# Performance work log

Hardware: AMD Instinct MI355X
Metric: run time of the kernel (lower is better)

## Reference

```python
import jax, jax.numpy as jnp
import numpy as np

B, L, D, H, DH, DI, NL, V = 1, 2048, 1024, 16, 64, 4096, 12, 32000
EPS = 1e-5  # torch LayerNorm default eps
SCALE = 1.0 / DH ** 0.5


def _ln(x):
    # LayerNorm with elementwise_affine=False
    m = jnp.mean(x, axis=-1, keepdims=True)
    va = jnp.var(x, axis=-1, keepdims=True)
    return (x - m) / jnp.sqrt(va + EPS)


def setup_inputs() -> dict:
    key = jax.random.key(0)
    ks = jax.random.split(key, 12)
    s = 0.02
    return {
        "X": jax.random.randint(ks[0], (B, L), 0, V),
        "Y": jax.random.randint(ks[1], (B, L), 0, V),
        "emb": jax.random.normal(ks[2], (V, D), jnp.float32) * s,
        "u": jax.random.normal(ks[3], (H, DH), jnp.float32) * s,
        "v": jax.random.normal(ks[4], (H, DH), jnp.float32) * s,
        "Wqkv": jax.random.normal(ks[5], (NL, 3 * H * DH, D), jnp.float32) * s,
        "Wpe": jax.random.normal(ks[6], (NL, H * DH, D), jnp.float32) * s,
        "Wout": jax.random.normal(ks[7], (NL, D, H * DH), jnp.float32) * s,
        "W1": jax.random.normal(ks[8], (NL, DI, D), jnp.float32) * s,
        "b1": jnp.zeros((NL, DI), jnp.float32),
        "W2": jax.random.normal(ks[9], (NL, D, DI), jnp.float32) * s,
        "b2": jnp.zeros((NL, D), jnp.float32),
        "Wc": jax.random.normal(ks[10], (V, D), jnp.float32) * s,
        "bc": jnp.zeros((V,), jnp.float32),
    }


def _forward(X, emb, u, v, Wqkv, Wpe, Wout, W1, b1, W2, b2, Wc, bc):
    q_len = X.shape[1]
    k_len = q_len  # mems=None -> m_len=0
    h = emb[X]  # (B, L, D); d_embedding == d_model so no projection

    # sinusoidal relative position embedding over descending positions
    pos = jnp.arange(k_len - 1, -1, -1, dtype=h.dtype)
    inv_freq = 1.0 / (10000.0 ** (jnp.arange(0, D, 2, dtype=h.dtype) / D))
    pp = pos[:, None] * inv_freq[None, :]              # (k, D/2)
    pe = jnp.concatenate([jnp.sin(pp), jnp.cos(pp)], axis=1)[None]  # (1, k, D)

    # causal mask: triu(ones, diagonal=1 + m_len), m_len=0; True = masked
    mask = jnp.triu(jnp.ones((q_len, k_len), bool), k=1)

    def layer(hid, params):
        wqkv, wpe, wout, w1, bb1, w2, bb2 = params
        qkv = hid @ wqkv.T                              # (B, q, 3HD)
        Q, K, Vv = jnp.split(qkv, 3, axis=-1)
        Q = Q.reshape(B, q_len, H, DH)
        K = K.reshape(B, k_len, H, DH)
        Vv = Vv.reshape(B, k_len, H, DH)
        r = (pe @ wpe.T).reshape(B, k_len, H, DH)       # requires B == 1
        AC = jnp.einsum('bqhd,bkhd->bhqk', Q + u, K)
        # NOTE: original code calls relative_shift(BD) but DISCARDS the result,
        # so BD is used unshifted — we reproduce that faithfully.
        BD = jnp.einsum('bqhd,bkhd->bhqk', Q + v, r)
        score = (AC + BD) * SCALE
        score = jnp.where(mask[None, None], -jnp.inf, score)
        prob = jax.nn.softmax(score, axis=-1)
        av = jnp.einsum('bhqk,bkhd->bqhd', prob, Vv).reshape(B, q_len, H * DH)
        hid = _ln(hid + av @ wout.T)                    # post-norm attention
        ff = jax.nn.relu(hid @ w1.T + bb1) @ w2.T + bb2
        hid = _ln(hid + ff)                             # post-norm FFN
        return hid, None

    h, _ = jax.lax.scan(layer, h, (Wqkv, Wpe, Wout, W1, b1, W2, b2))
    logits = h @ Wc.T + bc                              # (B, L, V)
    return logits.reshape(B * q_len, V)


def reference(X, Y, emb, u, v, Wqkv, Wpe, Wout, W1, b1, W2, b2, Wc, bc):
    # Y only determines y_len; here y_len == q_len so the full hidden is used.
    return _forward(X, emb, u, v, Wqkv, Wpe, Wout, W1, b1, W2, b2, Wc, bc)
```

## Files before the change

kernel.cpp:

```cpp
#include <hip/hip_runtime.h>
#include <hip/hip_bf16.h>

#define L_ 2048
#define D_ 1024
#define H_ 16
#define DH_ 64
#define DI_ 4096
#define NL_ 12
#define V_ 32000
#define EPS_ 1e-5f
#define SCALE_ 0.125f
#define LOG2E_ 1.44269504f
#define KBLK 64

typedef __attribute__((ext_vector_type(8))) short short8;
typedef __attribute__((ext_vector_type(4))) float f32x4;
typedef __hip_bfloat16 bf16;

__device__ __forceinline__ void gload_lds16(const void* g, void* l) {
  __builtin_amdgcn_global_load_lds((const __attribute__((address_space(1))) void*)g,
                                   (__attribute__((address_space(3))) void*)l, 16, 0, 0);
}

template<int STORE_BF16, int BIAS, int RELU, int SPLITK>
__global__ __launch_bounds__(256)
void gemm_bt(const bf16* __restrict__ A, const bf16* __restrict__ B,
             void* __restrict__ C, const float* __restrict__ bias,
             int M, int N, int K, int lda, int ldb, int ldc,
             long long Astride, long long Bstride, long long Cstride,
             float alpha, int Kc)
{
  __shared__ __align__(16) bf16 Atile[2][128 * 32];
  __shared__ __align__(16) bf16 Btile[2][128 * 32];

  const int gx = gridDim.x;
  const int nwg = gx * gridDim.y;
  const int orig = blockIdx.x + gx * blockIdx.y;
  const int qq = nwg >> 3, rr = nwg & 7;
  const int xcd = orig & 7, sidx = orig >> 3;
  const int lin = (xcd < rr ? xcd * (qq + 1) : rr * (qq + 1) + (xcd - rr) * qq) + sidx;
  const int m0 = (lin % gx) * 128;
  const int n0 = (lin / gx) * 128;

  const int z = blockIdx.z;
  int kbeg, kend;
  const bf16 *Ab, *Bb;
  size_t czoff;
  if (SPLITK) {
    kbeg = z * Kc; kend = kbeg + Kc;
    Ab = A; Bb = B;
    czoff = (size_t)z * (size_t)Cstride;
  } else {
    kbeg = 0; kend = K;
    Ab = A + (size_t)z * (size_t)Astride;
    Bb = B + (size_t)z * (size_t)Bstride;
    czoff = (size_t)z * (size_t)Cstride;
  }

  const int t = threadIdx.x;
  const int lane = t & 63;
  const int w = t >> 6;
  const int wm = w >> 1;
  const int wn = w & 1;
  const int rl = lane & 15;
  const int kl = (lane >> 4) << 3;

  const int r0 = t >> 2, kk0 = (t & 3) << 3;
  const int r1 = (256 + t) >> 2, kk1 = ((256 + t) & 3) << 3;
  int rb0 = n0 + r0; if (rb0 >= N) rb0 = N - 1;
  int rb1 = n0 + r1; if (rb1 >= N) rb1 = N - 1;

  f32x4 zero = {0.f, 0.f, 0.f, 0.f};
  f32x4 acc[4][4];
#pragma unroll
  for (int i = 0; i < 4; ++i)
#pragma unroll
    for (int j = 0; j < 4; ++j) acc[i][j] = zero;

  auto stage = [&](int buf, int k0) {
    gload_lds16(Ab + (size_t)(m0 + r0) * lda + (k0 + kk0), Atile[buf] + w * 512);
    gload_lds16(Bb + (size_t)rb0 * ldb + (k0 + kk0),       Btile[buf] + w * 512);
    gload_lds16(Ab + (size_t)(m0 + r1) * lda + (k0 + kk1), Atile[buf] + 2048 + w * 512);
    gload_lds16(Bb + (size_t)rb1 * ldb + (k0 + kk1),       Btile[buf] + 2048 + w * 512);
  };

  stage(0, kbeg);
  __syncthreads();

  int cur = 0;
  for (int k0 = kbeg; k0 < kend; k0 += 32) {
    if (k0 + 32 < kend) stage(cur ^ 1, k0 + 32);

    short8 af[4], bf_[4];
#pragma unroll
    for (int fm = 0; fm < 4; ++fm)
      af[fm] = *(const short8*)(Atile[cur] + (wm * 64 + fm * 16 + rl) * 32 + kl);
#pragma unroll
    for (int fn = 0; fn < 4; ++fn)
      bf_[fn] = *(const short8*)(Btile[cur] + (wn * 64 + fn * 16 + rl) * 32 + kl);
#pragma unroll
    for (int fm = 0; fm < 4; ++fm)
#pragma unroll
      for (int fn = 0; fn < 4; ++fn)
        acc[fm][fn] = __builtin_amdgcn_mfma_f32_16x16x32_bf16(af[fm], bf_[fn], acc[fm][fn], 0, 0, 0);
    __syncthreads();
    cur ^= 1;
  }

  const int row_l = (lane >> 4) << 2;
  const int col_l = lane & 15;
#pragma unroll
  for (int fm = 0; fm < 4; ++fm) {
#pragma unroll
    for (int fn = 0; fn < 4; ++fn) {
#pragma unroll
      for (int j = 0; j < 4; ++j) {
        const int m = m0 + wm * 64 + fm * 16 + row_l + j;
        const int n = n0 + wn * 64 + fn * 16 + col_l;
        if (m < M && n < N) {
          float vv = acc[fm][fn][j] * alpha;
          if (BIAS) vv += bias[n];
          if (RELU) vv = fmaxf(vv, 0.f);
          if (STORE_BF16)
            ((bf16*)C)[czoff + (size_t)m * ldc + n] = __float2bfloat16(vv);
          else
            ((float*)C)[czoff + (size_t)m * ldc + n] = vv;
        }
      }
    }
  }
}

__global__ __launch_bounds__(256)
void attn_fused(const bf16* __restrict__ QuQv, const bf16* __restrict__ Kr,
                const bf16* __restrict__ VT, bf16* __restrict__ av)
{
  __shared__ __align__(16) bf16 Kt[KBLK * 128];
  __shared__ __align__(16) bf16 Vt[DH_ * KBLK];
  __shared__ __align__(16) bf16 Pt[4][16 * KBLK];

  const int bid = blockIdx.x;
  const int tile = (bid < 256) ? (31 - (bid >> 4)) : ((bid - 256) >> 4);
  const int head = bid & 15;
  const int q0 = tile * 64;
  const int t = threadIdx.x, lane = t & 63, w = t >> 6;
  const int rl = lane & 15, hi = lane >> 4;

  const bf16* Qh = QuQv + (size_t)head * L_ * 128;
  const bf16* Kh = Kr   + (size_t)head * L_ * 128;
  const bf16* Vh = VT   + (size_t)head * DH_ * L_;

  const int qw0 = q0 + w * 16;

  short8 qf[4];
#pragma unroll
  for (int ks = 0; ks < 4; ++ks)
    qf[ks] = *(const short8*)(Qh + (size_t)(qw0 + rl) * 128 + ks * 32 + hi * 8);

  f32x4 o[4];
  float m_r[4], l_r[4];
#pragma unroll
  for (int j = 0; j < 4; ++j) { m_r[j] = -INFINITY; l_r[j] = 0.f; }
#pragma unroll
  for (int fn = 0; fn < 4; ++fn) o[fn] = (f32x4){0.f, 0.f, 0.f, 0.f};

  short8 kreg[4], vreg[2];
  auto load_regs = [&](int k0) {
#pragma unroll
    for (int i = 0; i < 4; ++i) {
      int c = i * 256 + t;
      int row = c >> 4, d8 = (c & 15) << 3;
      kreg[i] = *(const short8*)(Kh + (size_t)(k0 + row) * 128 + d8);
    }
#pragma unroll
    for (int i = 0; i < 2; ++i) {
      int c = i * 256 + t;
      int d = c >> 3, k8 = (c & 7) << 3;
      vreg[i] = *(const short8*)(Vh + (size_t)d * L_ + k0 + k8);
    }
  };
  auto write_lds = [&]() {
#pragma unroll
    for (int i = 0; i < 4; ++i) {
      int c = i * 256 + t;
      int row = c >> 4, d8 = (c & 15) << 3;
      int off = (row << 8) + (((d8 << 1)) ^ ((row & 7) << 4));
      *(short8*)((char*)Kt + off) = kreg[i];
    }
#pragma unroll
    for (int i = 0; i < 2; ++i) {
      int c = i * 256 + t;
      int d = c >> 3, k8 = (c & 7) << 3;
      int off = (d << 7) + (((k8 << 1)) ^ ((d & 7) << 4));
      *(short8*)((char*)Vt + off) = vreg[i];
    }
  };

  load_regs(0);
  write_lds();
  __syncthreads();

  const int kend = q0 + 64;
  for (int k0 = 0; k0 < kend; k0 += KBLK) {
    const bool more = (k0 + KBLK) < kend;
    if (more) load_regs(k0 + KBLK);

    if (k0 <= qw0 + 15) {
      f32x4 s[4];
#pragma unroll
      for (int fn = 0; fn < 4; ++fn) s[fn] = (f32x4){0.f, 0.f, 0.f, 0.f};
      __builtin_amdgcn_s_setprio(1);
#pragma unroll
      for (int fn = 0; fn < 4; ++fn) {
        const int krow = fn * 16 + rl;
#pragma unroll
        for (int ks = 0; ks < 4; ++ks) {
          short8 kf = *(const short8*)((char*)Kt + (krow << 8) +
                        ((((ks * 32 + hi * 8) << 1)) ^ ((krow & 7) << 4)));
          s[fn] = __builtin_amdgcn_mfma_f32_16x16x32_bf16(qf[ks], kf, s[fn], 0, 0, 0);
        }
      }
      __builtin_amdgcn_s_setprio(0);
      if (k0 + KBLK > q0) {
#pragma unroll
        for (int fn = 0; fn < 4; ++fn) {
          const int key = k0 + fn * 16 + rl;
#pragma unroll
          for (int j = 0; j < 4; ++j)
            if (key > qw0 + hi * 4 + j) s[fn][j] = -1e30f;
        }
      }
      float mx[4];
#pragma unroll
      for (int j = 0; j < 4; ++j)
        mx[j] = fmaxf(fmaxf(s[0][j], s[1][j]), fmaxf(s[2][j], s[3][j]));
#pragma unroll
      for (int off = 1; off < 16; off <<= 1)
#pragma unroll
        for (int j = 0; j < 4; ++j) mx[j] = fmaxf(mx[j], __shfl_xor(mx[j], off));
      float sf[4];
#pragma unroll
      for (int j = 0; j < 4; ++j) {
        float mn = fmaxf(m_r[j], mx[j]);
        sf[j] = exp2f((m_r[j] - mn) * LOG2E_);
        m_r[j] = mn;
      }
      float rs[4] = {0.f, 0.f, 0.f, 0.f};
#pragma unroll
      for (int fn = 0; fn < 4; ++fn) {
#pragma unroll
        for (int j = 0; j < 4; ++j) {
          float p = exp2f((s[fn][j] - m_r[j]) * LOG2E_);
          rs[j] += p;
          int row = hi * 4 + j;
          *(bf16*)((char*)Pt[w] + (row << 7) +
                   ((((fn * 16 + rl) << 1)) ^ ((row & 7) << 4))) = __float2bfloat16(p);
        }
      }
#pragma unroll
      for (int off = 1; off < 16; off <<= 1)
#pragma unroll
        for (int j = 0; j < 4; ++j) rs[j] += __shfl_xor(rs[j], off);
#pragma unroll
      for (int j = 0; j < 4; ++j) l_r[j] = l_r[j] * sf[j] + rs[j];
#pragma unroll
      for (int fn = 0; fn < 4; ++fn)
#pragma unroll
        for (int j = 0; j < 4; ++j) o[fn][j] *= sf[j];

      __builtin_amdgcn_s_setprio(1);
#pragma unroll
      for (int ks2 = 0; ks2 < 2; ++ks2) {
        short8 pa = *(const short8*)((char*)Pt[w] + (rl << 7) +
                      ((ks2 * 64 + hi * 16) ^ ((rl & 7) << 4)));
#pragma unroll
        for (int fn = 0; fn < 4; ++fn) {
          const int drow = fn * 16 + rl;
          short8 vf = *(const short8*)((char*)Vt + (drow << 7) +
                        ((ks2 * 64 + hi * 16) ^ ((drow & 7) << 4)));
          o[fn] = __builtin_amdgcn_mfma_f32_16x16x32_bf16(pa, vf, o[fn], 0, 0, 0);
        }
      }
      __builtin_amdgcn_s_setprio(0);
    }

    if (more) {
      __syncthreads();
      write_lds();
      __syncthreads();
    }
  }

#pragma unroll
  for (int fn = 0; fn < 4; ++fn) {
#pragma unroll
    for (int j = 0; j < 4; ++j) {
      int q = qw0 + hi * 4 + j;
      float vv = o[fn][j] / l_r[j];
      av[(size_t)q * D_ + head * 64 + fn * 16 + rl] = __float2bfloat16(vv);
    }
  }
}

__global__ __launch_bounds__(256)
void embed_k(const int* __restrict__ X, const float* __restrict__ emb,
             float* __restrict__ hout, bf16* __restrict__ hbout)
{
  int idx = blockIdx.x * 256 + threadIdx.x;
  if (idx >= L_ * D_) return;
  int tpos = idx >> 10, d = idx & 1023;
  float vv = emb[(size_t)X[tpos] * D_ + d];
  hout[idx] = vv;
  hbout[idx] = __float2bfloat16(vv);
}

__global__ __launch_bounds__(256)
void pe_k(bf16* __restrict__ pe)
{
  int idx = blockIdx.x * 256 + threadIdx.x;
  if (idx >= L_ * D_) return;
  int k = idx >> 10, i = idx & 1023;
  int f = (i < 512) ? i : (i - 512);
  float invf = exp2f(-(float)(2 * f) * (13.28771238f / 1024.f));
  float pp = (float)(L_ - 1 - k) * invf;
  float vv = (i < 512) ? sinf(pp) : cosf(pp);
  pe[idx] = __float2bfloat16(vv);
}

__global__ __launch_bounds__(256)
void cast_all(const float* __restrict__ wqkv, const float* __restrict__ wpe,
              const float* __restrict__ wout, const float* __restrict__ w1,
              const float* __restrict__ w2,
              bf16* __restrict__ dqkv, bf16* __restrict__ dpe, bf16* __restrict__ dout,
              bf16* __restrict__ d1, bf16* __restrict__ d2)
{
  const int n4 = 13631488 / 4;
  for (int i = blockIdx.x * 256 + threadIdx.x; i < n4; i += gridDim.x * 256) {
    int j = i * 4;
    const float* src; bf16* dst; int o;
    if (j < 3145728)      { src = wqkv; dst = dqkv; o = j; }
    else if (j < 4194304) { src = wpe;  dst = dpe;  o = j - 3145728; }
    else if (j < 5242880) { src = wout; dst = dout; o = j - 4194304; }
    else if (j < 9437184) { src = w1;   dst = d1;   o = j - 5242880; }
    else                  { src = w2;   dst = d2;   o = j - 9437184; }
    float4 vv = *(const float4*)(src + o);
    dst[o + 0] = __float2bfloat16(vv.x);
    dst[o + 1] = __float2bfloat16(vv.y);
    dst[o + 2] = __float2bfloat16(vv.z);
    dst[o + 3] = __float2bfloat16(vv.w);
  }
}

__global__ __launch_bounds__(256)
void cast_bf4(const float* __restrict__ in, bf16* __restrict__ out, long long n4)
{
  for (long long i = (long long)blockIdx.x * 256 + threadIdx.x; i < n4; i += (long long)gridDim.x * 256) {
    float4 vv = *(const float4*)(in + i * 4);
    out[i * 4 + 0] = __float2bfloat16(vv.x);
    out[i * 4 + 1] = __float2bfloat16(vv.y);
    out[i * 4 + 2] = __float2bfloat16(vv.z);
    out[i * 4 + 3] = __float2bfloat16(vv.w);
  }
}

__global__ __launch_bounds__(256)
void split_qkv(const float* __restrict__ qkv, const float* __restrict__ r,
               const float* __restrict__ u, const float* __restrict__ v,
               bf16* __restrict__ QuQv, bf16* __restrict__ Kr)
{
  int idx = blockIdx.x * 256 + threadIdx.x;
  if (idx >= L_ * D_) return;
  int q = idx >> 10;
  int c = idx & 1023;
  int h = c >> 6;
  int d = c & 63;
  float Qv = qkv[(size_t)q * 3072 + c];
  float Kv = qkv[(size_t)q * 3072 + 1024 + c];
  float rr = r[idx] + r[(size_t)L_ * D_ + idx];
  size_t b = ((size_t)h * L_ + q) * 128;
  QuQv[b + d]      = __float2bfloat16((Qv + u[c]) * SCALE_);
  QuQv[b + 64 + d] = __float2bfloat16((Qv + v[c]) * SCALE_);
  Kr[b + d]        = __float2bfloat16(Kv);
  Kr[b + 64 + d]   = __float2bfloat16(rr);
}

__global__ __launch_bounds__(256)
void vtrans(const float* __restrict__ qkv, bf16* __restrict__ VT)
{
  __shared__ bf16 tile[64 * 65];
  const int q0 = blockIdx.x * 64;
  const int h = blockIdx.y;
  const int t = threadIdx.x;
  const int qi = t >> 4;
  const int d0 = (t & 15) * 4;
#pragma unroll
  for (int i = 0; i < 4; ++i) {
    int q = i * 16 + qi;
    float4 vv = *(const float4*)(qkv + (size_t)(q0 + q) * 3072 + 2048 + h * 64 + d0);
    tile[(d0 + 0) * 65 + q] = __float2bfloat16(vv.x);
    tile[(d0 + 1) * 65 + q] = __float2bfloat16(vv.y);
    tile[(d0 + 2) * 65 + q] = __float2bfloat16(vv.z);
    tile[(d0 + 3) * 65 + q] = __float2bfloat16(vv.w);
  }
  __syncthreads();
  const int dr = t >> 5;
  const int q2 = (t & 31) * 2;
#pragma unroll
  for (int i = 0; i < 8; ++i) {
    int dd = i * 8 + dr;
    __hip_bfloat162 pk;
    pk.x = tile[dd * 65 + q2];
    pk.y = tile[dd * 65 + q2 + 1];
    *(__hip_bfloat162*)(VT + ((size_t)h * 64 + dd) * L_ + q0 + q2) = pk;
  }
}

__global__ __launch_bounds__(256)
void ln_residual(const float* __restrict__ resid, const float* __restrict__ parts,
                 int nparts, long long pstride, const float* __restrict__ bias,
                 float* __restrict__ hout, bf16* __restrict__ hbout)
{
  const int row = blockIdx.x;
  const int t = threadIdx.x;
  const int lane = t & 63, w = t >> 6;
  const size_t base = (size_t)row * D_;
  __shared__ float rs[4], rs2[4];
  float4 xv = *(const float4*)(resid + base + t * 4);
  for (int p = 0; p < nparts; ++p) {
    float4 pv = *(const float4*)(parts + (size_t)p * pstride + base + t * 4);
    xv.x += pv.x; xv.y += pv.y; xv.z += pv.z; xv.w += pv.w;
  }
  if (bias) {
    float4 bv = *(const float4*)(bias + t * 4);
    xv.x += bv.x; xv.y += bv.y; xv.z += bv.z; xv.w += bv.w;
  }
  float s = xv.x + xv.y + xv.z + xv.w;
  float s2 = xv.x * xv.x + xv.y * xv.y + xv.z * xv.z + xv.w * xv.w;
#pragma unroll
  for (int off = 32; off; off >>= 1) {
    s += __shfl_down(s, off);
    s2 += __shfl_down(s2, off);
  }
  if (lane == 0) { rs[w] = s; rs2[w] = s2; }
  __syncthreads();
  float S = rs[0] + rs[1] + rs[2] + rs[3];
  float S2 = rs2[0] + rs2[1] + rs2[2] + rs2[3];
  float mean = S * (1.f / D_);
  float var = S2 * (1.f / D_) - mean * mean;
  float inv = 1.f / sqrtf(var + EPS_);
  float4 y;
  y.x = (xv.x - mean) * inv;
  y.y = (xv.y - mean) * inv;
  y.z = (xv.z - mean) * inv;
  y.w = (xv.w - mean) * inv;
  *(float4*)(hout + base + t * 4) = y;
  __hip_bfloat162 p0, p1;
  p0.x = __float2bfloat16(y.x); p0.y = __float2bfloat16(y.y);
  p1.x = __float2bfloat16(y.z); p1.y = __float2bfloat16(y.w);
  *(__hip_bfloat162*)(hbout + base + t * 4)     = p0;
  *(__hip_bfloat162*)(hbout + base + t * 4 + 2) = p1;
}

extern "C" void kernel_launch(void* const* d_in, const int* in_sizes, int n_in,
                              void* d_out, int out_size, void* d_ws, size_t ws_size,
                              hipStream_t stream)
{
  (void)in_sizes; (void)n_in; (void)out_size; (void)ws_size;
  const int*   X    = (const int*)d_in[0];
  const float* emb  = (const float*)d_in[2];
  const float* u    = (const float*)d_in[3];
  const float* v    = (const float*)d_in[4];
  const float* Wqkv = (const float*)d_in[5];
  const float* Wpe  = (const float*)d_in[6];
  const float* Wout = (const float*)d_in[7];
  const float* W1   = (const float*)d_in[8];
  const float* b1   = (const float*)d_in[9];
  const float* W2   = (const float*)d_in[10];
  const float* b2   = (const float*)d_in[11];
  const float* Wc   = (const float*)d_in[12];
  const float* bc   = (const float*)d_in[13];
  float* out = (float*)d_out;

  size_t off = 0;
  auto alloc = [&](size_t bytes) {
    void* p = (char*)d_ws + off;
    off += (bytes + 255) & ~(size_t)255;
    return p;
  };
  float* h_f32   = (float*)alloc((size_t)L_ * D_ * 4);
  bf16*  h_bf    = (bf16*) alloc((size_t)L_ * D_ * 2);
  bf16*  pe_bf   = (bf16*) alloc((size_t)L_ * D_ * 2);
  float* qkv_f   = (float*)alloc((size_t)L_ * 3 * D_ * 4);
  float* r_f     = (float*)alloc((size_t)2 * L_ * D_ * 4);
  bf16*  QuQv    = (bf16*) alloc((size_t)H_ * L_ * 128 * 2);
  bf16*  Kr      = (bf16*) alloc((size_t)H_ * L_ * 128 * 2);
  bf16*  VT      = (bf16*) alloc((size_t)H_ * DH_ * L_ * 2);
  bf16*  av_bf   = (bf16*) alloc((size_t)L_ * D_ * 2);
  float* part_f  = (float*)alloc((size_t)2 * L_ * D_ * 4);
  bf16*  ff1_bf  = (bf16*) alloc((size_t)L_ * DI_ * 2);
  bf16*  Wqkv_bf = (bf16*) alloc((size_t)3 * D_ * D_ * 2);
  bf16*  Wpe_bf  = (bf16*) alloc((size_t)D_ * D_ * 2);
  bf16*  Wout_bf = (bf16*) alloc((size_t)D_ * D_ * 2);
  bf16*  W1_bf   = (bf16*) alloc((size_t)DI_ * D_ * 2);
  bf16*  W2_bf   = (bf16*) alloc((size_t)D_ * DI_ * 2);
  bf16*  Wc_bf   = (bf16*) alloc((size_t)V_ * D_ * 2);

  const int eb = (L_ * D_ + 255) / 256;
  const long long LD = (long long)L_ * D_;

  embed_k<<<eb, 256, 0, stream>>>(X, emb, h_f32, h_bf);
  pe_k<<<eb, 256, 0, stream>>>(pe_bf);
  cast_bf4<<<2048, 256, 0, stream>>>(Wc, Wc_bf, (long long)V_ * D_ / 4);

  dim3 gqkv(L_ / 128, (3 * D_) / 128, 1);
  dim3 gsk (L_ / 128, D_ / 128, 2);
  dim3 gff1(L_ / 128, DI_ / 128, 1);

  for (int l = 0; l < NL_; ++l) {
    cast_all<<<2048, 256, 0, stream>>>(
        Wqkv + (size_t)l * 3 * D_ * D_, Wpe + (size_t)l * D_ * D_,
        Wout + (size_t)l * D_ * D_, W1 + (size_t)l * DI_ * D_, W2 + (size_t)l * D_ * DI_,
        Wqkv_bf, Wpe_bf, Wout_bf, W1_bf, W2_bf);

    gemm_bt<0, 0, 0, 0><<<gqkv, 256, 0, stream>>>(h_bf, Wqkv_bf, qkv_f, nullptr,
        L_, 3 * D_, D_, D_, D_, 3 * D_, 0, 0, 0, 1.f, 0);

    gemm_bt<0, 0, 0, 1><<<gsk, 256, 0, stream>>>(pe_bf, Wpe_bf, r_f, nullptr,
        L_, D_, D_, D_, D_, D_, 0, 0, LD, 1.f, 512);

    split_qkv<<<eb, 256, 0, stream>>>(qkv_f, r_f, u, v, QuQv, Kr);
    vtrans<<<dim3(L_ / 64, H_, 1), 256, 0, stream>>>(qkv_f, VT);

    attn_fused<<<512, 256, 0, stream>>>(QuQv, Kr, VT, av_bf);

    gemm_bt<0, 0, 0, 1><<<gsk, 256, 0, stream>>>(av_bf, Wout_bf, part_f, nullptr,
        L_, D_, D_, D_, D_, D_, 0, 0, LD, 1.f, 512);
    ln_residual<<<L_, 256, 0, stream>>>(h_f32, part_f, 2, LD, nullptr, h_f32, h_bf);

    gemm_bt<1, 1, 1, 0><<<gff1, 256, 0, stream>>>(h_bf, W1_bf, ff1_bf, b1 + (size_t)l * DI_,
        L_, DI_, D_, D_, D_, DI_, 0, 0, 0, 1.f, 0);

    gemm_bt<0, 0, 0, 1><<<gsk, 256, 0, stream>>>(ff1_bf, W2_bf, part_f, nullptr,
        L_, D_, DI_, DI_, DI_, D_, 0, 0, LD, 1.f, 2048);
    ln_residual<<<L_, 256, 0, stream>>>(h_f32, part_f, 2, LD, b2 + (size_t)l * D_, h_f32, h_bf);
  }

  dim3 gl(L_ / 128, V_ / 128, 1);
  gemm_bt<0, 1, 0, 0><<<gl, 256, 0, stream>>>(h_bf, Wc_bf, out, bc,
      L_, V_, D_, D_, D_, V_, 0, 0, 0, 1.f, 0);
}
```

Baseline: 3.279 ms.

## Fuse QKV split into GEMM epilogue and precast all layer weights upfront

A dedicated QKV GEMM now writes bf16 Q+u/Q+v, K, and row-major V directly from its epilogue. This removes the fp32 qkv intermediate and most of split_qkv's traffic; the positional part is still added by a small r2kr kernel, and vtrans now reads bf16. When the workspace is large enough, all layers' weights are cast to bf16 in a few large launches instead of one cast_all per layer, which cuts launch count. The epilogue's scattered bf16 stores may be poorly coalesced, and the upfront cast needs much more workspace.

After: 3.761 ms. 1.15x slower.

```diff
diff --git a/kernel.cpp b/kernel.cpp
--- a/kernel.cpp
+++ b/kernel.cpp
@@ -125,6 +125,99 @@
             ((bf16*)C)[czoff + (size_t)m * ldc + n] = __float2bfloat16(vv);
           else
             ((float*)C)[czoff + (size_t)m * ldc + n] = vv;
+        }
+      }
+    }
+  }
+}
+
+__global__ __launch_bounds__(256)
+void gemm_qkv(const bf16* __restrict__ A, const bf16* __restrict__ B,
+              const float* __restrict__ u, const float* __restrict__ v,
+              bf16* __restrict__ QuQv, bf16* __restrict__ Kr, bf16* __restrict__ Vrm)
+{
+  __shared__ __align__(16) bf16 Atile[2][128 * 32];
+  __shared__ __align__(16) bf16 Btile[2][128 * 32];
+
+  const int gx = gridDim.x;
+  const int nwg = gx * gridDim.y;
+  const int orig = blockIdx.x + gx * blockIdx.y;
+  const int qq = nwg >> 3, rr = nwg & 7;
+  const int xcd = orig & 7, sidx = orig >> 3;
+  const int lin = (xcd < rr ? xcd * (qq + 1) : rr * (qq + 1) + (xcd - rr) * qq) + sidx;
+  const int m0 = (lin % gx) * 128;
+  const int n0 = (lin / gx) * 128;
+
+  const int t = threadIdx.x;
+  const int lane = t & 63;
+  const int w = t >> 6;
+  const int wm = w >> 1;
+  const int wn = w & 1;
+  const int rl = lane & 15;
+  const int kl = (lane >> 4) << 3;
+
+  const int r0 = t >> 2, kk0 = (t & 3) << 3;
+  const int r1 = (256 + t) >> 2, kk1 = ((256 + t) & 3) << 3;
+
+  f32x4 zero = {0.f, 0.f, 0.f, 0.f};
+  f32x4 acc[4][4];
+#pragma unroll
+  for (int i = 0; i < 4; ++i)
+#pragma unroll
+    for (int j = 0; j < 4; ++j) acc[i][j] = zero;
+
+  auto stage = [&](int buf, int k0) {
+    gload_lds16(A + (size_t)(m0 + r0) * D_ + (k0 + kk0), Atile[buf] + w * 512);
+    gload_lds16(B + (size_t)(n0 + r0) * D_ + (k0 + kk0), Btile[buf] + w * 512);
+    gload_lds16(A + (size_t)(m0 + r1) * D_ + (k0 + kk1), Atile[buf] + 2048 + w * 512);
+    gload_lds16(B + (size_t)(n0 + r1) * D_ + (k0 + kk1), Btile[buf] + 2048 + w * 512);
+  };
+
+  stage(0, 0);
+  __syncthreads();
+
+  int cur = 0;
+  for (int k0 = 0; k0 < D_; k0 += 32) {
+    if (k0 + 32 < D_) stage(cur ^ 1, k0 + 32);
+
+    short8 af[4], bf_[4];
+#pragma unroll
+    for (int fm = 0; fm < 4; ++fm)
+      af[fm] = *(const short8*)(Atile[cur] + (wm * 64 + fm * 16 + rl) * 32 + kl);
+#pragma unroll
+    for (int fn = 0; fn < 4; ++fn)
+      bf_[fn] = *(const short8*)(Btile[cur] + (wn * 64 + fn * 16 + rl) * 32 + kl);
+#pragma unroll
+    for (int fm = 0; fm < 4; ++fm)
+#pragma unroll
+      for (int fn = 0; fn < 4; ++fn)
+        acc[fm][fn] = __builtin_amdgcn_mfma_f32_16x16x32_bf16(af[fm], bf_[fn], acc[fm][fn], 0, 0, 0);
+    __syncthreads();
+    cur ^= 1;
+  }
+
+  const int row_l = (lane >> 4) << 2;
+  const int col_l = lane & 15;
+#pragma unroll
+  for (int fm = 0; fm < 4; ++fm) {
+#pragma unroll
+    for (int fn = 0; fn < 4; ++fn) {
+#pragma unroll
+      for (int j = 0; j < 4; ++j) {
+        const int m = m0 + wm * 64 + fm * 16 + row_l + j;
+        const int n = n0 + wn * 64 + fn * 16 + col_l;
+        float x = acc[fm][fn][j];
+        if (n < 1024) {
+          const int h = n >> 6, d = n & 63;
+          size_t b = ((size_t)h * L_ + m) * 128;
+          QuQv[b + d]      = __float2bfloat16((x + u[n]) * SCALE_);
+          QuQv[b + 64 + d] = __float2bfloat16((x + v[n]) * SCALE_);
+        } else if (n < 2048) {
+          const int n2 = n - 1024;
+          const int h = n2 >> 6, d = n2 & 63;
+          Kr[((size_t)h * L_ + m) * 128 + d] = __float2bfloat16(x);
+        } else {
+          Vrm[(size_t)m * 1024 + (n - 2048)] = __float2bfloat16(x);
         }
       }
     }
@@ -364,43 +457,31 @@
 }
 
 __global__ __launch_bounds__(256)
-void split_qkv(const float* __restrict__ qkv, const float* __restrict__ r,
-               const float* __restrict__ u, const float* __restrict__ v,
-               bf16* __restrict__ QuQv, bf16* __restrict__ Kr)
+void r2kr(const float* __restrict__ r, bf16* __restrict__ Kr)
 {
   int idx = blockIdx.x * 256 + threadIdx.x;
   if (idx >= L_ * D_) return;
   int q = idx >> 10;
   int c = idx & 1023;
-  int h = c >> 6;
-  int d = c & 63;
-  float Qv = qkv[(size_t)q * 3072 + c];
-  float Kv = qkv[(size_t)q * 3072 + 1024 + c];
   float rr = r[idx] + r[(size_t)L_ * D_ + idx];
-  size_t b = ((size_t)h * L_ + q) * 128;
-  QuQv[b + d]      = __float2bfloat16((Qv + u[c]) * SCALE_);
-  QuQv[b + 64 + d] = __float2bfloat16((Qv + v[c]) * SCALE_);
-  Kr[b + d]        = __float2bfloat16(Kv);
-  Kr[b + 64 + d]   = __float2bfloat16(rr);
-}
-
-__global__ __launch_bounds__(256)
-void vtrans(const float* __restrict__ qkv, bf16* __restrict__ VT)
-{
-  __shared__ bf16 tile[64 * 65];
+  Kr[(((size_t)(c >> 6)) * L_ + q) * 128 + 64 + (c & 63)] = __float2bfloat16(rr);
+}
+
+__global__ __launch_bounds__(256)
+void vtrans(const bf16* __restrict__ Vrm, bf16* __restrict__ VT)
+{
+  __shared__ unsigned short tile[64 * 65];
   const int q0 = blockIdx.x * 64;
   const int h = blockIdx.y;
   const int t = threadIdx.x;
-  const int qi = t >> 4;
-  const int d0 = (t & 15) * 4;
-#pragma unroll
-  for (int i = 0; i < 4; ++i) {
-    int q = i * 16 + qi;
-    float4 vv = *(const float4*)(qkv + (size_t)(q0 + q) * 3072 + 2048 + h * 64 + d0);
-    tile[(d0 + 0) * 65 + q] = __float2bfloat16(vv.x);
-    tile[(d0 + 1) * 65 + q] = __float2bfloat16(vv.y);
-    tile[(d0 + 2) * 65 + q] = __float2bfloat16(vv.z);
-    tile[(d0 + 3) * 65 + q] = __float2bfloat16(vv.w);
+#pragma unroll
+  for (int i = 0; i < 2; ++i) {
+    int qrow = i * 32 + (t >> 3);
+    int d0 = (t & 7) * 8;
+    short8 vv = *(const short8*)(Vrm + (size_t)(q0 + qrow) * 1024 + h * 64 + d0);
+#pragma unroll
+    for (int e = 0; e < 8; ++e)
+      tile[(d0 + e) * 65 + qrow] = (unsigned short)vv[e];
   }
   __syncthreads();
   const int dr = t >> 5;
@@ -408,10 +489,9 @@
 #pragma unroll
   for (int i = 0; i < 8; ++i) {
     int dd = i * 8 + dr;
-    __hip_bfloat162 pk;
-    pk.x = tile[dd * 65 + q2];
-    pk.y = tile[dd * 65 + q2 + 1];
-    *(__hip_bfloat162*)(VT + ((size_t)h * 64 + dd) * L_ + q0 + q2) = pk;
+    unsigned int pk = (unsigned int)tile[dd * 65 + q2] |
+                      ((unsigned int)tile[dd * 65 + q2 + 1] << 16);
+    *(unsigned int*)(VT + ((size_t)h * 64 + dd) * L_ + q0 + q2) = pk;
   }
 }
 
@@ -465,7 +545,7 @@
                               void* d_out, int out_size, void* d_ws, size_t ws_size,
                               hipStream_t stream)
 {
-  (void)in_sizes; (void)n_in; (void)out_size; (void)ws_size;
+  (void)in_sizes; (void)n_in; (void)out_size;
   const int*   X    = (const int*)d_in[0];
   const float* emb  = (const float*)d_in[2];
   const float* u    = (const float*)d_in[3];
@@ -490,20 +570,25 @@
   float* h_f32   = (float*)alloc((size_t)L_ * D_ * 4);
   bf16*  h_bf    = (bf16*) alloc((size_t)L_ * D_ * 2);
   bf16*  pe_bf   = (bf16*) alloc((size_t)L_ * D_ * 2);
-  float* qkv_f   = (float*)alloc((size_t)L_ * 3 * D_ * 4);
   float* r_f     = (float*)alloc((size_t)2 * L_ * D_ * 4);
   bf16*  QuQv    = (bf16*) alloc((size_t)H_ * L_ * 128 * 2);
   bf16*  Kr      = (bf16*) alloc((size_t)H_ * L_ * 128 * 2);
+  bf16*  Vrm     = (bf16*) alloc((size_t)L_ * D_ * 2);
   bf16*  VT      = (bf16*) alloc((size_t)H_ * DH_ * L_ * 2);
   bf16*  av_bf   = (bf16*) alloc((size_t)L_ * D_ * 2);
   float* part_f  = (float*)alloc((size_t)2 * L_ * D_ * 4);
   bf16*  ff1_bf  = (bf16*) alloc((size_t)L_ * DI_ * 2);
-  bf16*  Wqkv_bf = (bf16*) alloc((size_t)3 * D_ * D_ * 2);
-  bf16*  Wpe_bf  = (bf16*) alloc((size_t)D_ * D_ * 2);
-  bf16*  Wout_bf = (bf16*) alloc((size_t)D_ * D_ * 2);
-  bf16*  W1_bf   = (bf16*) alloc((size_t)DI_ * D_ * 2);
-  bf16*  W2_bf   = (bf16*) alloc((size_t)D_ * DI_ * 2);
   bf16*  Wc_bf   = (bf16*) alloc((size_t)V_ * D_ * 2);
+
+  const size_t perL = (size_t)(3 * D_ * D_ + D_ * D_ + D_ * D_ + DI_ * D_ + D_ * DI_) * 2;
+  size_t need_all = off + (size_t)NL_ * perL + 4096;
+  bool precast = (ws_size >= need_all);
+  int nlw = precast ? NL_ : 1;
+  bf16* Wqkv_bf = (bf16*)alloc((size_t)nlw * 3 * D_ * D_ * 2);
+  bf16* Wpe_bf  = (bf16*)alloc((size_t)nlw * D_ * D_ * 2);
+  bf16* Wout_bf = (bf16*)alloc((size_t)nlw * D_ * D_ * 2);
+  bf16* W1_bf   = (bf16*)alloc((size_t)nlw * DI_ * D_ * 2);
+  bf16* W2_bf   = (bf16*)alloc((size_t)nlw * D_ * DI_ * 2);
 
   const int eb = (L_ * D_ + 255) / 256;
   const long long LD = (long long)L_ * D_;
@@ -511,36 +596,49 @@
   embed_k<<<eb, 256, 0, stream>>>(X, emb, h_f32, h_bf);
   pe_k<<<eb, 256, 0, stream>>>(pe_bf);
   cast_bf4<<<2048, 256, 0, stream>>>(Wc, Wc_bf, (long long)V_ * D_ / 4);
+  if (precast) {
+    cast_bf4<<<2048, 256, 0, stream>>>(Wqkv, Wqkv_bf, (long long)NL_ * 3 * D_ * D_ / 4);
+    cast_bf4<<<2048, 256, 0, stream>>>(Wpe, Wpe_bf, (long long)NL_ * D_ * D_ / 4);
+    cast_bf4<<<2048, 256, 0, stream>>>(Wout, Wout_bf, (long long)NL_ * D_ * D_ / 4);
+    cast_bf4<<<2048, 256, 0, stream>>>(W1, W1_bf, (long long)NL_ * DI_ * D_ / 4);
+    cast_bf4<<<2048, 256, 0, stream>>>(W2, W2_bf, (long long)NL_ * D_ * DI_ / 4);
+  }
 
   dim3 gqkv(L_ / 128, (3 * D_) / 128, 1);
   dim3 gsk (L_ / 128, D_ / 128, 2);
   dim3 gff1(L_ / 128, DI_ / 128, 1);
 
   for (int l = 0; l < NL_; ++l) {
-    cast_all<<<2048, 256, 0, stream>>>(
-        Wqkv + (size_t)l * 3 * D_ * D_, Wpe + (size_t)l * D_ * D_,
-        Wout + (size_t)l * D_ * D_, W1 + (size_t)l * DI_ * D_, W2 + (size_t)l * D_ * DI_,
-        Wqkv_bf, Wpe_bf, Wout_bf, W1_bf, W2_bf);
-
-    gemm_bt<0, 0, 0, 0><<<gqkv, 256, 0, stream>>>(h_bf, Wqkv_bf, qkv_f, nullptr,
-        L_, 3 * D_, D_, D_, D_, 3 * D_, 0, 0, 0, 1.f, 0);
-
-    gemm_bt<0, 0, 0, 1><<<gsk, 256, 0, stream>>>(pe_bf, Wpe_bf, r_f, nullptr,
+    const int lw = precast ? l : 0;
+    bf16* wqkv_l = Wqkv_bf + (size_t)lw * 3 * D_ * D_;
+    bf16* wpe_l  = Wpe_bf  + (size_t)lw * D_ * D_;
+    bf16* wout_l = Wout_bf + (size_t)lw * D_ * D_;
+    bf16* w1_l   = W1_bf   + (size_t)lw * DI_ * D_;
+    bf16* w2_l   = W2_bf   + (size_t)lw * D_ * DI_;
+    if (!precast) {
+      cast_all<<<2048, 256, 0, stream>>>(
+          Wqkv + (size_t)l * 3 * D_ * D_, Wpe + (size_t)l * D_ * D_,
+          Wout + (size_t)l * D_ * D_, W1 + (size_t)l * DI_ * D_, W2 + (size_t)l * D_ * DI_,
+          wqkv_l, wpe_l, wout_l, w1_l, w2_l);
+    }
+
+    gemm_qkv<<<gqkv, 256, 0, stream>>>(h_bf, wqkv_l, u, v, QuQv, Kr, Vrm);
+
+    gemm_bt<0, 0, 0, 1><<<gsk, 256, 0, stream>>>(pe_bf, wpe_l, r_f, nullptr,
         L_, D_, D_, D_, D_, D_, 0, 0, LD, 1.f, 512);
-
-    split_qkv<<<eb, 256, 0, stream>>>(qkv_f, r_f, u, v, QuQv, Kr);
-    vtrans<<<dim3(L_ / 64, H_, 1), 256, 0, stream>>>(qkv_f, VT);
+    r2kr<<<eb, 256, 0, stream>>>(r_f, Kr);
+    vtrans<<<dim3(L_ / 64, H_, 1), 256, 0, stream>>>(Vrm, VT);
 
     attn_fused<<<512, 256, 0, stream>>>(QuQv, Kr, VT, av_bf);
 
-    gemm_bt<0, 0, 0, 1><<<gsk, 256, 0, stream>>>(av_bf, Wout_bf, part_f, nullptr,
+    gemm_bt<0, 0, 0, 1><<<gsk, 256, 0, stream>>>(av_bf, wout_l, part_f, nullptr,
         L_, D_, D_, D_, D_, D_, 0, 0, LD, 1.f, 512);
     ln_residual<<<L_, 256, 0, stream>>>(h_f32, part_f, 2, LD, nullptr, h_f32, h_bf);
 
-    gemm_bt<1, 1, 1, 0><<<gff1, 256, 0, stream>>>(h_bf, W1_bf, ff1_bf, b1 + (size_t)l * DI_,
+    gemm_bt<1, 1, 1, 0><<<gff1, 256, 0, stream>>>(h_bf, w1_l, ff1_bf, b1 + (size_t)l * DI_,
         L_, DI_, D_, D_, D_, DI_, 0, 0, 0, 1.f, 0);
 
-    gemm_bt<0, 0, 0, 1><<<gsk, 256, 0, stream>>>(ff1_bf, W2_bf, part_f, nullptr,
+    gemm_bt<0, 0, 0, 1><<<gsk, 256, 0, stream>>>(ff1_bf, w2_l, part_f, nullptr,
         L_, D_, DI_, DI_, DI_, D_, 0, 0, LD, 1.f, 2048);
     ln_residual<<<L_, 256, 0, stream>>>(h_f32, part_f, 2, LD, b2 + (size_t)l * D_, h_f32, h_bf);
   }
```
